# Kernel tuning notes

Hardware: AMD Instinct MI355X
Metric: run time of the kernel (lower is better)

## Reference

```python
import jax, jax.numpy as jnp
import numpy as np

ALPHA, GAMMA = 0.25, 2.0
IOU_THRES = 0.5
WEIGHTS = (10.0, 10.0, 5.0, 5.0, 15.0)
MAXV = 16  # max polygon verts during quad-vs-quad clipping (<=8, padded)


def box_corners(b):
    # b: (5,) = cx, cy, w, h, theta(rad); returns (4,2) CCW corners
    cx, cy, w, h, t = b[0], b[1], b[2], b[3], b[4]
    c, s = jnp.cos(t), jnp.sin(t)
    dx = jnp.array([-0.5, 0.5, 0.5, -0.5]) * w
    dy = jnp.array([-0.5, -0.5, 0.5, 0.5]) * h
    return jnp.stack([cx + dx * c - dy * s, cy + dx * s + dy * c], axis=-1)


def pair_iou(b1, b2):
    # exact rotated-rectangle IoU via Sutherland-Hodgman clipping
    p1 = box_corners(b1)
    p2 = box_corners(b2)
    poly = jnp.zeros((MAXV, 2)).at[:4].set(p1)
    n = jnp.int32(4)
    for e in range(4):
        a = p2[e]
        d = p2[(e + 1) % 4] - a
        out = jnp.zeros((MAXV, 2))
        m = jnp.int32(0)
        for i in range(MAXV):
            cur = poly[i]
            nxt = poly[jnp.where(i + 1 >= n, 0, i + 1)]
            sc = d[0] * (cur[1] - a[1]) - d[1] * (cur[0] - a[0])
            sn = d[0] * (nxt[1] - a[1]) - d[1] * (nxt[0] - a[0])
            valid = i < n
            keep = valid & (sc >= 0)
            out = out.at[m].set(jnp.where(keep, cur, out[m]))
            m = m + keep.astype(jnp.int32)
            crossed = valid & ((sc >= 0) != (sn >= 0))
            den = sc - sn
            t = sc / jnp.where(den == 0, 1.0, den)
            ip = cur + t * (nxt - cur)
            out = out.at[m].set(jnp.where(crossed, ip, out[m]))
            m = m + crossed.astype(jnp.int32)
        poly, n = out, m
    idx = jnp.arange(MAXV)
    nxt = jnp.where(idx + 1 >= n, 0, idx + 1)
    cr = poly[:, 0] * poly[nxt, 1] - poly[nxt, 0] * poly[:, 1]
    inter = 0.5 * jnp.abs(jnp.sum(jnp.where(idx < n, cr, 0.0)))
    union = b1[2] * b1[3] + b2[2] * b2[3] - inter
    return inter / jnp.maximum(union, 1e-9)


rbox_iou_mat = jax.vmap(jax.vmap(pair_iou, (None, 0)), (0, None))  # (A,5),(G,5)->(A,G)


def min_area_square(rb):
    s = jnp.maximum(rb[:, 2], rb[:, 3])
    return jnp.stack([rb[:, 0] - s / 2, rb[:, 1] - s / 2,
                      rb[:, 0] + s / 2, rb[:, 1] + s / 2], 1)


def bbox_overlaps(a, b):
    lt = jnp.maximum(a[:, None, :2], b[None, :, :2])
    rb = jnp.minimum(a[:, None, 2:], b[None, :, 2:])
    wh = jnp.clip(rb - lt, 0.0)
    inter = wh[..., 0] * wh[..., 1]
    aa = (a[:, 2] - a[:, 0]) * (a[:, 3] - a[:, 1])
    ab = (b[:, 2] - b[:, 0]) * (b[:, 3] - b[:, 1])
    return inter / jnp.maximum(aa[:, None] + ab[None, :] - inter, 1e-9)


def encode(ex, gt):
    wx, wy, ww, wh, wt = WEIGHTS
    ew = jnp.maximum(ex[:, 2], 1.0); eh = jnp.maximum(ex[:, 3], 1.0)
    gw = jnp.maximum(gt[:, 2], 1.0); gh = jnp.maximum(gt[:, 3], 1.0)
    dx = wx * (gt[:, 0] - ex[:, 0]) / ew
    dy = wy * (gt[:, 1] - ex[:, 1]) / eh
    dw = ww * jnp.log(gw / ew)
    dh = wh * jnp.log(gh / eh)
    dt = wt * (jnp.tan(gt[:, 4]) - jnp.tan(ex[:, 4]))
    return jnp.stack([dx, dy, dw, dh, dt], 1)


def lmr5pangle(anch, dt):
    # encoded angle offset of the 90-degree-swapped box: tan(t+pi/2) = -1/tan(t)
    wt = WEIGHTS[4]
    ta = jnp.tan(anch[:, 4])
    tg = dt / wt + ta
    tg = jnp.where(jnp.abs(tg) < 1e-4, jnp.where(tg < 0, -1e-4, 1e-4), tg)
    return wt * (-1.0 / tg - ta)


def landmark_encode(ex, lm):
    wx, wy = WEIGHTS[0], WEIGHTS[1]
    ew = jnp.maximum(ex[:, 2], 1.0); eh = jnp.maximum(ex[:, 3], 1.0)
    return jnp.stack([wx * (lm[:, 0] - ex[:, 0]) / ew,
                      wy * (lm[:, 1] - ex[:, 1]) / eh,
                      wx * (lm[:, 2] - ex[:, 0]) / ew,
                      wy * (lm[:, 3] - ex[:, 1]) / eh], 1)


def smooth_l1(d, beta=1.0 / 9):
    d = jnp.abs(d)
    return jnp.where(d < beta, 0.5 * d * d / beta, d - 0.5 * beta)


def lmr5p_per_anchor(pred, tgt, anch):
    t22 = lmr5pangle(anch, pred[:, 4])
    l1 = smooth_l1(tgt[:, 0] - pred[:, 0])
    l2 = smooth_l1(tgt[:, 1] - pred[:, 1])
    l3 = smooth_l1(tgt[:, 2] - pred[:, 2])
    l4 = smooth_l1(tgt[:, 3] - pred[:, 3])
    l5 = smooth_l1(tgt[:, 2] - pred[:, 3])  # |w1 - h2|
    l6 = smooth_l1(tgt[:, 3] - pred[:, 2])  # |h1 - w2|
    l7 = smooth_l1(tgt[:, 4] - pred[:, 4])
    l8 = smooth_l1(tgt[:, 4] - t22)
    return jnp.minimum(l1 + l2 + l3 + l4 + l7, l1 + l2 + l5 + l6 + l8)


def balanced_l1(d, beta=0.5, al=0.5, ga=0.9):
    d = jnp.abs(d)
    b = np.e ** (ga / al) - 1.0
    return jnp.where(d < beta,
                     al / b * (b * d + 1.0) * jnp.log(b * d / beta + 1.0) - al * d,
                     ga * d + ga / b - al * beta)


def per_image(cls, reg, lmk, anch, ann, ls):
    valid_g = ann[:, -1] != -1.0
    has_gt = jnp.any(valid_g)
    cls = jnp.clip(cls, 1e-4, 1.0 - 1e-4)
    indicator = bbox_overlaps(min_area_square(anch), min_area_square(ann[:, :5]))
    riou = rbox_iou_mat(anch, ann[:, :5])
    ious = jnp.where(indicator >= 0.1, riou, 0.0)   # rbox_overlaps thresh=0.1 gating
    ious = jnp.where(valid_g[None, :], ious, -1.0)  # mask padded gts
    ious = jax.lax.stop_gradient(ious)              # torch computes ious on cpu numpy
    iou_max = ious.max(1)
    iou_argmax = ious.argmax(1)
    pos = iou_max >= IOU_THRES
    max_gt = ious.max(0)
    argmax_gt = ious.argmax(0)
    force = valid_g & (max_gt < IOU_THRES)
    pos = (pos.astype(jnp.int32).at[argmax_gt].max(force.astype(jnp.int32))) > 0
    num_pos = pos.sum()
    denom = jnp.maximum(num_pos.astype(cls.dtype), 1.0)
    assigned = ann[iou_argmax]                       # (A, 6)
    lab = assigned[:, -1].astype(jnp.int32)
    onehot = (lab[:, None] == jnp.arange(cls.shape[-1])[None, :]).astype(cls.dtype)
    tgt = jnp.where(pos[:, None], onehot,
                    jnp.where((iou_max < IOU_THRES - 0.1)[:, None], 0.0, -1.0))
    af = jnp.where(tgt == 1.0, ALPHA, 1.0 - ALPHA)
    fw = af * jnp.where(tgt == 1.0, 1.0 - cls, cls) ** GAMMA
    bce = -(tgt * jnp.log(cls + 1e-6) + (1.0 - tgt) * jnp.log(1.0 - cls + 1e-6))
    cls_loss = jnp.where(tgt != -1.0, fw * bce, 0.0).sum() / denom
    cls_loss = jnp.where(has_gt, cls_loss, 0.0)
    gt_safe = jnp.where(pos[:, None], assigned[:, :5], anch)  # keep masked lanes finite
    tg1 = encode(anch, gt_safe)
    r1 = jnp.where(pos, lmr5p_per_anchor(reg, tg1, anch), 0.0).sum() / (5.0 * denom)
    r1 = jnp.where(has_gt & (num_pos > 0), r1, 0.0)
    lm_safe = jnp.where(pos[:, None], ls[iou_argmax],
                        jnp.stack([anch[:, 0], anch[:, 1], anch[:, 0], anch[:, 1]], 1))
    tg2 = landmark_encode(anch, lm_safe)
    r2 = jnp.where(pos[:, None], balanced_l1(lmk - tg2), 0.0).sum() / (4.0 * denom)
    r2 = jnp.where(has_gt & (num_pos > 0), r2, 0.0)
    return cls_loss, r1, r2


def setup_inputs() -> dict:
    B, A, G, C = 2, 16384, 24, 8
    NV = 16  # valid gts per image; remaining rows padded with label -1
    ks = jax.random.split(jax.random.key(0), 16)
    classifications = jax.random.uniform(ks[0], (B, A, C), jnp.float32)
    regressions = jax.random.normal(ks[1], (B, A, 5), jnp.float32) * 0.1
    landmarks = jax.random.normal(ks[2], (B, A, 4), jnp.float32) * 0.1
    gcx = 100.0 + 800.0 * jax.random.uniform(ks[3], (B, G))
    gcy = 100.0 + 800.0 * jax.random.uniform(ks[4], (B, G))
    gw = 40.0 + 160.0 * jax.random.uniform(ks[5], (B, G))
    gh = 40.0 + 160.0 * jax.random.uniform(ks[6], (B, G))
    gth = 1.2 * jax.random.uniform(ks[7], (B, G)) - 0.6
    lab = jax.random.randint(ks[8], (B, G), 0, C).astype(jnp.float32)
    lab = jnp.where(jnp.arange(G)[None, :] >= NV, -1.0, lab)
    annotations = jnp.stack([gcx, gcy, gw, gh, gth, lab], -1)
    acx = 1024.0 * jax.random.uniform(ks[9], (B, A))
    acy = 1024.0 * jax.random.uniform(ks[10], (B, A))
    aw = 16.0 + 112.0 * jax.random.uniform(ks[11], (B, A))
    ah = 16.0 + 112.0 * jax.random.uniform(ks[12], (B, A))
    ath = 1.2 * jax.random.uniform(ks[13], (B, A)) - 0.6
    anchors = jnp.stack([acx, acy, aw, ah, ath], -1)
    # plant jittered copies of the gts so a healthy number of anchors are positive
    jit = jax.random.normal(ks[14], (B, G, 5)) * jnp.array([2.0, 2.0, 2.0, 2.0, 0.01])
    anchors = anchors.at[:, :G, :].set(annotations[:, :, :5] + jit)
    ca, sa = jnp.cos(gth), jnp.sin(gth)
    gt_linestrips = jnp.stack([gcx - 0.4 * gw * ca, gcy - 0.4 * gw * sa,
                               gcx + 0.4 * gw * ca, gcy + 0.4 * gw * sa], -1)
    return {"classifications": classifications, "regressions": regressions,
            "anchors": anchors, "annotations": annotations,
            "landmarks": landmarks, "gt_linestrips": gt_linestrips}


def reference(classifications, regressions, anchors, annotations, landmarks, gt_linestrips):
    cls_l, r1, r2 = jax.vmap(per_image)(classifications, regressions, landmarks,
                                        anchors, annotations, gt_linestrips)
    return (cls_l.mean(keepdims=True), r1.mean(keepdims=True), r2.mean(keepdims=True))
```

## Files before the change

kernel.cpp:

```cpp
#include <hip/hip_runtime.h>
#include <math.h>

#define B_N 2
#define A_N 16384
#define G_N 24
#define C_N 8
#define NV  16
#define BPI 256

#define OFF_GTKEY  0
#define OFF_AKEY   384
#define OFF_PART   (384 + B_N * A_N * 8)

__device__ inline unsigned int fmap(float v) {
    unsigned int u = __float_as_uint(v);
    return (u & 0x80000000u) ? ~u : (u | 0x80000000u);
}
__device__ inline float funmap(unsigned int u) {
    unsigned int bits = (u & 0x80000000u) ? (u ^ 0x80000000u) : ~u;
    return __uint_as_float(bits);
}
__device__ inline unsigned long long mkkey(float v, int idx) {
    return ((unsigned long long)fmap(v) << 32) |
           (unsigned long long)(0xFFFFFFFFu - (unsigned int)idx);
}
__device__ inline float key_val(unsigned long long k) { return funmap((unsigned int)(k >> 32)); }
__device__ inline int   key_idx(unsigned long long k) { return (int)(0xFFFFFFFFu - (unsigned int)k); }

__device__ inline float smoothl1(float x) {
    const float beta = 1.0f / 9.0f;
    float d = fabsf(x);
    return (d < beta) ? (0.5f * d * d / beta) : (d - 0.5f * beta);
}
__device__ inline float balancedl1(float x) {
    const float bb  = 5.049647464412945f;
    const float alb = 0.5f / 5.049647464412945f;
    const float gab = 0.9f / 5.049647464412945f;
    float d = fabsf(x);
    if (d < 0.5f)
        return alb * (bb * d + 1.0f) * logf(bb * d / 0.5f + 1.0f) - 0.5f * d;
    return 0.9f * d + gab - 0.25f;
}
__device__ inline float focal_pos(const float* cr, int lab) {
    float s = 0.0f;
#pragma unroll
    for (int c = 0; c < C_N; c++) {
        float p = fminf(fmaxf(cr[c], 1e-4f), 0.9999f);
        if (c == lab) s += 0.25f * (1.0f - p) * (1.0f - p) * (-logf(p + 1e-6f));
        else          s += 0.75f * p * p * (-logf(1.0f - p + 1e-6f));
    }
    return s;
}
__device__ inline float focal_neg(const float* cr) {
    float s = 0.0f;
#pragma unroll
    for (int c = 0; c < C_N; c++) {
        float p = fminf(fmaxf(cr[c], 1e-4f), 0.9999f);
        s += 0.75f * p * p * (-logf(1.0f - p + 1e-6f));
    }
    return s;
}
__device__ inline float reg_loss(const float* rr, const float* ar, const float* annr) {
    float acx = ar[0], acy = ar[1], aw = ar[2], ah = ar[3], ath = ar[4];
    float aw1 = fmaxf(aw, 1.0f), ah1 = fmaxf(ah, 1.0f);
    float gw1 = fmaxf(annr[2], 1.0f), gh1 = fmaxf(annr[3], 1.0f);
    float t1 = 10.0f * (annr[0] - acx) / aw1;
    float t2 = 10.0f * (annr[1] - acy) / ah1;
    float t3 = 5.0f * logf(gw1 / aw1);
    float t4 = 5.0f * logf(gh1 / ah1);
    float ta = tanf(ath);
    float t5 = 15.0f * (tanf(annr[4]) - ta);
    float p0 = rr[0], p1 = rr[1], p2 = rr[2], p3 = rr[3], p4 = rr[4];
    float tg = p4 / 15.0f + ta;
    if (fabsf(tg) < 1e-4f) tg = (tg < 0.0f) ? -1e-4f : 1e-4f;
    float t22 = 15.0f * (-1.0f / tg - ta);
    float l1 = smoothl1(t1 - p0), l2 = smoothl1(t2 - p1);
    float l3 = smoothl1(t3 - p2), l4 = smoothl1(t4 - p3);
    float l5 = smoothl1(t3 - p3), l6 = smoothl1(t4 - p2);
    float l7 = smoothl1(t5 - p4), l8 = smoothl1(t5 - t22);
    return fminf(l1 + l2 + l3 + l4 + l7, l1 + l2 + l5 + l6 + l8);
}
__device__ inline float lmk_loss(const float* lk, const float* ar, const float* lr) {
    float acx = ar[0], acy = ar[1];
    float aw1 = fmaxf(ar[2], 1.0f), ah1 = fmaxf(ar[3], 1.0f);
    return balancedl1(lk[0] - 10.0f * (lr[0] - acx) / aw1)
         + balancedl1(lk[1] - 10.0f * (lr[1] - acy) / ah1)
         + balancedl1(lk[2] - 10.0f * (lr[2] - acx) / aw1)
         + balancedl1(lk[3] - 10.0f * (lr[3] - acy) / ah1);
}

__global__ __launch_bounds__(64) void k_main(
    const float* __restrict__ cls, const float* __restrict__ reg,
    const float* __restrict__ anch, const float* __restrict__ ann,
    const float* __restrict__ lmk, const float* __restrict__ ls,
    unsigned long long* __restrict__ gtkey, unsigned long long* __restrict__ akey,
    float* __restrict__ partials)
{
    __shared__ float pb[2][2][NV][64];
    __shared__ float gcor[G_N][10];
    __shared__ float gsq[G_N][5];
    __shared__ float glab[G_N];

    const int tid = threadIdx.x;
    const int b   = blockIdx.x >> 8;
    const int a   = ((blockIdx.x & (BPI - 1)) << 6) | tid;
    const size_t idx = (size_t)b * A_N + a;
    const float* annb = ann + (size_t)b * G_N * 6;

    if (tid < G_N) {
        const float* annr = annb + tid * 6;
        float gcx = annr[0], gcy = annr[1], gw = annr[2], gh = annr[3], gth = annr[4];
        glab[tid] = annr[5];
        float sg = fmaxf(gw, gh);
        float gx1 = gcx - sg * 0.5f, gy1 = gcy - sg * 0.5f;
        float gx2 = gcx + sg * 0.5f, gy2 = gcy + sg * 0.5f;
        gsq[tid][0] = gx1; gsq[tid][1] = gy1; gsq[tid][2] = gx2; gsq[tid][3] = gy2;
        gsq[tid][4] = (gx2 - gx1) * (gy2 - gy1);
        float c2 = cosf(gth), s2 = sinf(gth);
        const float dxs[4] = {-0.5f, 0.5f, 0.5f, -0.5f};
        const float dys[4] = {-0.5f, -0.5f, 0.5f, 0.5f};
#pragma unroll
        for (int k = 0; k < 4; k++) {
            float ex = dxs[k] * gw, ey = dys[k] * gh;
            gcor[tid][k]     = gcx + ex * c2 - ey * s2;
            gcor[tid][4 + k] = gcy + ex * s2 + ey * c2;
        }
        gcor[tid][8] = gw * gh;
    }
    if (a == 0) {
        for (int g = 0; g < G_N; g++)
            atomicMax(&gtkey[b * G_N + g], mkkey(0.0f, 0));
    }
    __syncthreads();

    unsigned int validmask = 0;
    for (int g = 0; g < G_N; g++)
        if (glab[g] != -1.0f) validmask |= (1u << g);
    int first_valid = validmask ? (__ffs((int)validmask) - 1) : -1;

    const float* ar = anch + idx * 5;
    float acx = ar[0], acy = ar[1], aw = ar[2], ah = ar[3], ath = ar[4];

    float sa = fmaxf(aw, ah);
    float ax1 = acx - sa * 0.5f, ay1 = acy - sa * 0.5f;
    float ax2 = acx + sa * 0.5f, ay2 = acy + sa * 0.5f;
    float areaA = (ax2 - ax1) * (ay2 - ay1);

    unsigned int mask = 0;
    for (unsigned int vm = validmask; vm; vm &= vm - 1) {
        int g = __ffs((int)vm) - 1;
        float gx1 = gsq[g][0], gy1 = gsq[g][1], gx2 = gsq[g][2], gy2 = gsq[g][3];
        float iw = fmaxf(fminf(ax2, gx2) - fmaxf(ax1, gx1), 0.0f);
        float ih = fmaxf(fminf(ay2, gy2) - fmaxf(ay1, gy1), 0.0f);
        float inter0 = iw * ih;
        float ind = inter0 / fmaxf(areaA + gsq[g][4] - inter0, 1e-9f);
        if (ind >= 0.1f) mask |= (1u << g);
    }

    float c1 = cosf(ath), s1 = sinf(ath);
    float axk[4], ayk[4];
    {
        const float dxs[4] = {-0.5f, 0.5f, 0.5f, -0.5f};
        const float dys[4] = {-0.5f, -0.5f, 0.5f, 0.5f};
#pragma unroll
        for (int k = 0; k < 4; k++) {
            float dx = dxs[k] * aw, dy = dys[k] * ah;
            axk[k] = acx + dx * c1 - dy * s1;
            ayk[k] = acy + dx * s1 + dy * c1;
        }
    }
    float areaWH = aw * ah;

    unsigned long long rowkey = (first_valid >= 0) ? mkkey(0.0f, first_valid) : 0ull;

    while (__any(mask != 0)) {
        if (mask) {
            int g = __ffs((int)mask) - 1;
            mask &= mask - 1;
            float p2x[4], p2y[4];
#pragma unroll
            for (int k = 0; k < 4; k++) {
                p2x[k] = gcor[g][k];
                p2y[k] = gcor[g][4 + k];
                pb[0][0][k][tid] = axk[k];
                pb[0][1][k][tid] = ayk[k];
            }
            int n = 4, cb = 0;
#pragma unroll
            for (int e = 0; e < 4; e++) {
                float apx = p2x[e], apy = p2y[e];
                float dx = p2x[(e + 1) & 3] - apx, dy = p2y[(e + 1) & 3] - apy;
                int m = 0, nb = cb ^ 1;
                for (int i = 0; i < n; i++) {
                    float cx_ = pb[cb][0][i][tid], cy_ = pb[cb][1][i][tid];
                    int j = (i + 1 >= n) ? 0 : (i + 1);
                    float nx_ = pb[cb][0][j][tid], ny_ = pb[cb][1][j][tid];
                    float sc = dx * (cy_ - apy) - dy * (cx_ - apx);
                    float sn = dx * (ny_ - apy) - dy * (nx_ - apx);
                    bool ci = (sc >= 0.0f), niv = (sn >= 0.0f);
                    if (ci) {
                        if (m < NV) { pb[nb][0][m][tid] = cx_; pb[nb][1][m][tid] = cy_; }
                        m++;
                    }
                    if (ci != niv) {
                        float den = sc - sn;
                        float t = sc / ((den == 0.0f) ? 1.0f : den);
                        if (m < NV) {
                            pb[nb][0][m][tid] = cx_ + t * (nx_ - cx_);
                            pb[nb][1][m][tid] = cy_ + t * (ny_ - cy_);
                        }
                        m++;
                    }
                }
                n = (m > NV) ? NV : m;
                cb = nb;
            }
            float ssum = 0.0f;
            for (int i = 0; i < n; i++) {
                int j = (i + 1 >= n) ? 0 : (i + 1);
                ssum += pb[cb][0][i][tid] * pb[cb][1][j][tid]
                      - pb[cb][0][j][tid] * pb[cb][1][i][tid];
            }
            float interA = 0.5f * fabsf(ssum);
            float uni = areaWH + gcor[g][8] - interA;
            float val = interA / fmaxf(uni, 1e-9f);

            unsigned long long k = mkkey(val, g);
            if (k > rowkey) rowkey = k;
            if (val > 0.0f) atomicMax(&gtkey[b * G_N + g], mkkey(val, a));
        }
    }

    akey[idx] = rowkey;

    float iou_max = key_val(rowkey);
    int gmax = key_idx(rowkey);
    const float* annr = annb + gmax * 6;
    const float* cr = cls + idx * C_N;
    float cls_sum = 0.0f, reg_sum = 0.0f, lmk_sum = 0.0f;
    int pc = 0;
    if (iou_max >= 0.5f) {
        pc = 1;
        cls_sum = focal_pos(cr, (int)annr[5]);
        reg_sum = reg_loss(reg + idx * 5, ar, annr);
        lmk_sum = lmk_loss(lmk + idx * 4, ar, ls + (size_t)(b * G_N + gmax) * 4);
    } else if (iou_max < 0.4f) {
        cls_sum = focal_neg(cr);
    }

    float fpc = (float)pc;
    for (int off = 32; off; off >>= 1) {
        cls_sum += __shfl_down(cls_sum, off);
        reg_sum += __shfl_down(reg_sum, off);
        lmk_sum += __shfl_down(lmk_sum, off);
        fpc     += __shfl_down(fpc, off);
    }
    if (tid == 0) {
        float* p = partials + (size_t)blockIdx.x * 4;
        p[0] = cls_sum; p[1] = reg_sum; p[2] = lmk_sum; p[3] = fpc;
    }
}

__global__ __launch_bounds__(128) void k_fix(
    const float* __restrict__ cls, const float* __restrict__ reg,
    const float* __restrict__ anch, const float* __restrict__ ann,
    const float* __restrict__ lmk, const float* __restrict__ ls,
    const unsigned long long* __restrict__ gtkey, const unsigned long long* __restrict__ akey,
    const float* __restrict__ partials, float* __restrict__ out)
{
    __shared__ float res[B_N][3];
    const int tid = threadIdx.x;
    const int b = tid >> 6, lane = tid & 63;

    double s0 = 0.0, s1 = 0.0, s2 = 0.0, s3 = 0.0;
    for (int r = lane; r < BPI; r += 64) {
        const float* p = partials + (size_t)(b * BPI + r) * 4;
        s0 += p[0]; s1 += p[1]; s2 += p[2]; s3 += p[3];
    }
    for (int off = 32; off; off >>= 1) {
        s0 += __shfl_down(s0, off);
        s1 += __shfl_down(s1, off);
        s2 += __shfl_down(s2, off);
        s3 += __shfl_down(s3, off);
    }

    const float* annb = ann + (size_t)b * G_N * 6;
    float dc = 0.0f, dr = 0.0f, dl = 0.0f; int dn = 0;
    if (lane < G_N) {
        bool valid = annb[lane * 6 + 5] != -1.0f;
        unsigned long long k = gtkey[b * G_N + lane];
        int fa = key_idx(k);
        bool force = valid && (key_val(k) < 0.5f);
        if (force) {
            for (int g2 = 0; g2 < lane; g2++) {
                if (annb[g2 * 6 + 5] == -1.0f) continue;
                unsigned long long k2 = gtkey[b * G_N + g2];
                if (key_val(k2) < 0.5f && key_idx(k2) == fa) { force = false; break; }
            }
        }
        if (force) {
            size_t fidx = (size_t)b * A_N + fa;
            unsigned long long ak = akey[fidx];
            float im = key_val(ak);
            if (!(im >= 0.5f)) {
                dn = 1;
                int gm = key_idx(ak);
                const float* cr = cls + fidx * C_N;
                const float* annr = annb + gm * 6;
                const float* arr = anch + fidx * 5;
                dc = focal_pos(cr, (int)annr[5]);
                if (im < 0.4f) dc -= focal_neg(cr);
                dr = reg_loss(reg + fidx * 5, arr, annr);
                dl = lmk_loss(lmk + fidx * 4, arr, ls + (size_t)(b * G_N + gm) * 4);
            }
        }
    }
    float fdn = (float)dn;
    for (int off = 32; off; off >>= 1) {
        dc  += __shfl_down(dc, off);
        dr  += __shfl_down(dr, off);
        dl  += __shfl_down(dl, off);
        fdn += __shfl_down(fdn, off);
    }
    if (lane == 0) {
        bool has_gt = false;
        for (int g = 0; g < G_N; g++)
            if (annb[g * 6 + 5] != -1.0f) has_gt = true;
        float np = (float)s3 + fdn;
        float denom = fmaxf(np, 1.0f);
        res[b][0] = has_gt ? (float)((s0 + dc) / denom) : 0.0f;
        res[b][1] = (has_gt && np > 0.0f) ? (float)((s1 + dr) / (5.0 * denom)) : 0.0f;
        res[b][2] = (has_gt && np > 0.0f) ? (float)((s2 + dl) / (4.0 * denom)) : 0.0f;
    }
    __syncthreads();
    if (tid == 0) {
        out[0] = (res[0][0] + res[1][0]) * 0.5f;
        out[1] = (res[0][1] + res[1][1]) * 0.5f;
        out[2] = (res[0][2] + res[1][2]) * 0.5f;
    }
}

extern "C" void kernel_launch(void* const* d_in, const int* in_sizes, int n_in,
                              void* d_out, int out_size, void* d_ws, size_t ws_size,
                              hipStream_t stream)
{
    (void)in_sizes; (void)n_in; (void)out_size; (void)ws_size;
    const float* cls  = (const float*)d_in[0];
    const float* reg  = (const float*)d_in[1];
    const float* anch = (const float*)d_in[2];
    const float* ann  = (const float*)d_in[3];
    const float* lmk  = (const float*)d_in[4];
    const float* ls   = (const float*)d_in[5];

    char* ws = (char*)d_ws;
    unsigned long long* gtkey = (unsigned long long*)(ws + OFF_GTKEY);
    unsigned long long* akey  = (unsigned long long*)(ws + OFF_AKEY);
    float* partials = (float*)(ws + OFF_PART);
    float* out = (float*)d_out;

    hipMemsetAsync(gtkey, 0, B_N * G_N * 8, stream);
    hipLaunchKernelGGL(k_main, dim3(B_N * BPI), dim3(64), 0, stream,
                       cls, reg, anch, ann, lmk, ls, gtkey, akey, partials);
    hipLaunchKernelGGL(k_fix, dim3(1), dim3(128), 0, stream,
                       cls, reg, anch, ann, lmk, ls, gtkey, akey, partials, out);
}
```

Baseline: 103.2 us.

## Compact candidate anchor-gt pairs into a shared worklist for balanced clipping

Instead of each thread looping over its own candidate gts, which leaves lanes idle while the lane with the most candidates finishes, the prefilter now appends every passing (anchor, gt) pair to a shared worklist built with a ballot and prefix count. The 64 threads then work through that list evenly, reading anchor corners from shared memory and combining each row's maximum with a shared-memory atomicMax. Classification logits are also loaded into registers at the start of the kernel so that global load latency overlaps with the setup work. In exchange it adds shared-memory atomics, extra barriers and more shared memory per block.

```diff
diff --git a/kernel.cpp b/kernel.cpp
--- a/kernel.cpp
+++ b/kernel.cpp
@@ -100,12 +100,23 @@
     __shared__ float gcor[G_N][10];
     __shared__ float gsq[G_N][5];
     __shared__ float glab[G_N];
+    __shared__ float acor[9][64];
+    __shared__ unsigned long long rowk[64];
+    __shared__ unsigned short wl[G_N * 64];
 
     const int tid = threadIdx.x;
     const int b   = blockIdx.x >> 8;
     const int a   = ((blockIdx.x & (BPI - 1)) << 6) | tid;
     const size_t idx = (size_t)b * A_N + a;
     const float* annb = ann + (size_t)b * G_N * 6;
+
+    const float* cr = cls + idx * C_N;
+    float crv[C_N];
+#pragma unroll
+    for (int c = 0; c < C_N; c++) crv[c] = cr[c];
+
+    const float* ar = anch + idx * 5;
+    float acx = ar[0], acy = ar[1], aw = ar[2], ah = ar[3], ath = ar[4];
 
     if (tid < G_N) {
         const float* annr = annb + tid * 6;
@@ -131,6 +142,19 @@
         for (int g = 0; g < G_N; g++)
             atomicMax(&gtkey[b * G_N + g], mkkey(0.0f, 0));
     }
+
+    {
+        float c1 = cosf(ath), s1 = sinf(ath);
+        const float dxs[4] = {-0.5f, 0.5f, 0.5f, -0.5f};
+        const float dys[4] = {-0.5f, -0.5f, 0.5f, 0.5f};
+#pragma unroll
+        for (int k = 0; k < 4; k++) {
+            float dx = dxs[k] * aw, dy = dys[k] * ah;
+            acor[k][tid]     = acx + dx * c1 - dy * s1;
+            acor[4 + k][tid] = acy + dx * s1 + dy * c1;
+        }
+        acor[8][tid] = aw * ah;
+    }
     __syncthreads();
 
     unsigned int validmask = 0;
@@ -138,15 +162,14 @@
         if (glab[g] != -1.0f) validmask |= (1u << g);
     int first_valid = validmask ? (__ffs((int)validmask) - 1) : -1;
 
-    const float* ar = anch + idx * 5;
-    float acx = ar[0], acy = ar[1], aw = ar[2], ah = ar[3], ath = ar[4];
+    rowk[tid] = (first_valid >= 0) ? mkkey(0.0f, first_valid) : 0ull;
 
     float sa = fmaxf(aw, ah);
     float ax1 = acx - sa * 0.5f, ay1 = acy - sa * 0.5f;
     float ax2 = acx + sa * 0.5f, ay2 = acy + sa * 0.5f;
     float areaA = (ax2 - ax1) * (ay2 - ay1);
 
-    unsigned int mask = 0;
+    int cnt = 0;
     for (unsigned int vm = validmask; vm; vm &= vm - 1) {
         int g = __ffs((int)vm) - 1;
         float gx1 = gsq[g][0], gy1 = gsq[g][1], gx2 = gsq[g][2], gy2 = gsq[g][3];
@@ -154,98 +177,91 @@
         float ih = fmaxf(fminf(ay2, gy2) - fmaxf(ay1, gy1), 0.0f);
         float inter0 = iw * ih;
         float ind = inter0 / fmaxf(areaA + gsq[g][4] - inter0, 1e-9f);
-        if (ind >= 0.1f) mask |= (1u << g);
-    }
-
-    float c1 = cosf(ath), s1 = sinf(ath);
-    float axk[4], ayk[4];
-    {
-        const float dxs[4] = {-0.5f, 0.5f, 0.5f, -0.5f};
-        const float dys[4] = {-0.5f, -0.5f, 0.5f, 0.5f};
+        bool pass = (ind >= 0.1f);
+        unsigned long long bal = __ballot(pass);
+        if (pass) {
+            int off = __popcll(bal & ((1ull << tid) - 1ull));
+            wl[cnt + off] = (unsigned short)((tid << 5) | g);
+        }
+        cnt += __popcll(bal);
+    }
+    __syncthreads();
+
+    for (int i = tid; i < cnt; i += 64) {
+        unsigned int e = wl[i];
+        int owner = (int)(e >> 5);
+        int g = (int)(e & 31u);
+        float p2x[4], p2y[4];
 #pragma unroll
         for (int k = 0; k < 4; k++) {
-            float dx = dxs[k] * aw, dy = dys[k] * ah;
-            axk[k] = acx + dx * c1 - dy * s1;
-            ayk[k] = acy + dx * s1 + dy * c1;
-        }
-    }
-    float areaWH = aw * ah;
-
-    unsigned long long rowkey = (first_valid >= 0) ? mkkey(0.0f, first_valid) : 0ull;
-
-    while (__any(mask != 0)) {
-        if (mask) {
-            int g = __ffs((int)mask) - 1;
-            mask &= mask - 1;
-            float p2x[4], p2y[4];
-#pragma unroll
-            for (int k = 0; k < 4; k++) {
-                p2x[k] = gcor[g][k];
-                p2y[k] = gcor[g][4 + k];
-                pb[0][0][k][tid] = axk[k];
-                pb[0][1][k][tid] = ayk[k];
+            p2x[k] = gcor[g][k];
+            p2y[k] = gcor[g][4 + k];
+            pb[0][0][k][tid] = acor[k][owner];
+            pb[0][1][k][tid] = acor[4 + k][owner];
+        }
+        int n = 4, cb = 0;
+#pragma unroll
+        for (int e4 = 0; e4 < 4; e4++) {
+            float apx = p2x[e4], apy = p2y[e4];
+            float dx = p2x[(e4 + 1) & 3] - apx, dy = p2y[(e4 + 1) & 3] - apy;
+            int m = 0, nb = cb ^ 1;
+            for (int i2 = 0; i2 < n; i2++) {
+                float cx_ = pb[cb][0][i2][tid], cy_ = pb[cb][1][i2][tid];
+                int j = (i2 + 1 >= n) ? 0 : (i2 + 1);
+                float nx_ = pb[cb][0][j][tid], ny_ = pb[cb][1][j][tid];
+                float sc = dx * (cy_ - apy) - dy * (cx_ - apx);
+                float sn = dx * (ny_ - apy) - dy * (nx_ - apx);
+                bool ci = (sc >= 0.0f), niv = (sn >= 0.0f);
+                if (ci) {
+                    if (m < NV) { pb[nb][0][m][tid] = cx_; pb[nb][1][m][tid] = cy_; }
+                    m++;
+                }
+                if (ci != niv) {
+                    float den = sc - sn;
+                    float t = sc / ((den == 0.0f) ? 1.0f : den);
+                    if (m < NV) {
+                        pb[nb][0][m][tid] = cx_ + t * (nx_ - cx_);
+                        pb[nb][1][m][tid] = cy_ + t * (ny_ - cy_);
+                    }
+                    m++;
+                }
             }
-            int n = 4, cb = 0;
-#pragma unroll
-            for (int e = 0; e < 4; e++) {
-                float apx = p2x[e], apy = p2y[e];
-                float dx = p2x[(e + 1) & 3] - apx, dy = p2y[(e + 1) & 3] - apy;
-                int m = 0, nb = cb ^ 1;
-                for (int i = 0; i < n; i++) {
-                    float cx_ = pb[cb][0][i][tid], cy_ = pb[cb][1][i][tid];
-                    int j = (i + 1 >= n) ? 0 : (i + 1);
-                    float nx_ = pb[cb][0][j][tid], ny_ = pb[cb][1][j][tid];
-                    float sc = dx * (cy_ - apy) - dy * (cx_ - apx);
-                    float sn = dx * (ny_ - apy) - dy * (nx_ - apx);
-                    bool ci = (sc >= 0.0f), niv = (sn >= 0.0f);
-                    if (ci) {
-                        if (m < NV) { pb[nb][0][m][tid] = cx_; pb[nb][1][m][tid] = cy_; }
-                        m++;
-                    }
-                    if (ci != niv) {
-                        float den = sc - sn;
-                        float t = sc / ((den == 0.0f) ? 1.0f : den);
-                        if (m < NV) {
-                            pb[nb][0][m][tid] = cx_ + t * (nx_ - cx_);
-                            pb[nb][1][m][tid] = cy_ + t * (ny_ - cy_);
-                        }
-                        m++;
-                    }
-                }
-                n = (m > NV) ? NV : m;
-                cb = nb;
-            }
-            float ssum = 0.0f;
-            for (int i = 0; i < n; i++) {
-                int j = (i + 1 >= n) ? 0 : (i + 1);
-                ssum += pb[cb][0][i][tid] * pb[cb][1][j][tid]
-                      - pb[cb][0][j][tid] * pb[cb][1][i][tid];
-            }
-            float interA = 0.5f * fabsf(ssum);
-            float uni = areaWH + gcor[g][8] - interA;
-            float val = interA / fmaxf(uni, 1e-9f);
-
-            unsigned long long k = mkkey(val, g);
-            if (k > rowkey) rowkey = k;
-            if (val > 0.0f) atomicMax(&gtkey[b * G_N + g], mkkey(val, a));
-        }
-    }
-
+            n = (m > NV) ? NV : m;
+            cb = nb;
+        }
+        float ssum = 0.0f;
+        for (int i2 = 0; i2 < n; i2++) {
+            int j = (i2 + 1 >= n) ? 0 : (i2 + 1);
+            ssum += pb[cb][0][i2][tid] * pb[cb][1][j][tid]
+                  - pb[cb][0][j][tid] * pb[cb][1][i2][tid];
+        }
+        float interA = 0.5f * fabsf(ssum);
+        float uni = acor[8][owner] + gcor[g][8] - interA;
+        float val = interA / fmaxf(uni, 1e-9f);
+
+        atomicMax(&rowk[owner], mkkey(val, g));
+        if (val > 0.0f) {
+            int aowner = ((blockIdx.x & (BPI - 1)) << 6) | owner;
+            atomicMax(&gtkey[b * G_N + g], mkkey(val, aowner));
+        }
+    }
+    __syncthreads();
+
+    unsigned long long rowkey = rowk[tid];
     akey[idx] = rowkey;
 
     float iou_max = key_val(rowkey);
     int gmax = key_idx(rowkey);
     const float* annr = annb + gmax * 6;
-    const float* cr = cls + idx * C_N;
     float cls_sum = 0.0f, reg_sum = 0.0f, lmk_sum = 0.0f;
     int pc = 0;
     if (iou_max >= 0.5f) {
         pc = 1;
-        cls_sum = focal_pos(cr, (int)annr[5]);
+        cls_sum = focal_pos(crv, (int)annr[5]);
         reg_sum = reg_loss(reg + idx * 5, ar, annr);
         lmk_sum = lmk_loss(lmk + idx * 4, ar, ls + (size_t)(b * G_N + gmax) * 4);
     } else if (iou_max < 0.4f) {
-        cls_sum = focal_neg(cr);
+        cls_sum = focal_neg(crv);
     }
 
     float fpc = (float)pc;
@@ -306,10 +322,13 @@
                 dn = 1;
                 int gm = key_idx(ak);
                 const float* cr = cls + fidx * C_N;
+                float crv[C_N];
+#pragma unroll
+                for (int c = 0; c < C_N; c++) crv[c] = cr[c];
                 const float* annr = annb + gm * 6;
                 const float* arr = anch + fidx * 5;
-                dc = focal_pos(cr, (int)annr[5]);
-                if (im < 0.4f) dc -= focal_neg(cr);
+                dc = focal_pos(crv, (int)annr[5]);
+                if (im < 0.4f) dc -= focal_neg(crv);
                 dr = reg_loss(reg + fidx * 5, arr, annr);
                 dl = lmk_loss(lmk + fidx * 4, arr, ls + (size_t)(b * G_N + gm) * 4);
             }
```

Measured after the change: 103.9 us. Within noise of the previous version (+0.7%).
